# Kernel optimization log

Hardware: AMD Instinct MI355X
Metric: run time of the kernel (lower is better)

The kernel has to match this reference:

```python
import jax, jax.numpy as jnp
import numpy as np

N_NODES = 10000
N_PAIRS = 200000
NUM_FEATURES = 384
DEGREES = [1, 2, 3]
NHEADS = len(DEGREES)
F_HEAD = NUM_FEATURES // NHEADS  # 128
REPEATS = np.array([2 * d + 1 for d in DEGREES])  # [3,5,7]
SPH_DIM = int(REPEATS.sum())  # 15


def setup_inputs() -> dict:
    key = jax.random.key(0)
    ks = jax.random.split(key, 10)
    return {
        "chi": jax.random.normal(ks[0], (N_NODES, SPH_DIM), dtype=jnp.float32),
        "sph_ij": jax.random.normal(ks[1], (N_PAIRS, SPH_DIM), dtype=jnp.float32),
        "x": jax.random.normal(ks[2], (N_NODES, NUM_FEATURES), dtype=jnp.float32),
        "w_ij": jax.random.normal(ks[3], (N_PAIRS, NUM_FEATURES), dtype=jnp.float32),
        "idx_i": jax.random.randint(ks[4], (N_PAIRS,), 0, N_NODES),
        "phi_r_cut": jax.random.uniform(ks[5], (N_PAIRS, 1), dtype=jnp.float32),
        "phi_chi_cut": jax.random.uniform(ks[6], (N_PAIRS,), dtype=jnp.float32),
        "idx_j": jax.random.randint(ks[7], (N_PAIRS,), 0, N_NODES),
        # per-head linear weights (nn.Linear stores (out, in); y = x @ W.T)
        "Wq": jax.random.normal(ks[8], (NHEADS, F_HEAD, F_HEAD), dtype=jnp.float32) / np.sqrt(F_HEAD),
        "Wk": jax.random.normal(ks[9], (NHEADS, F_HEAD, F_HEAD), dtype=jnp.float32) / np.sqrt(F_HEAD),
    }


def reference(chi, sph_ij, x, w_ij, idx_i, phi_r_cut, phi_chi_cut, idx_j, Wq, Wk):
    n = x.shape[0]
    # split into heads: (n, H, Fh) / (E, H, Fh)
    x_h = x.reshape(n, NHEADS, F_HEAD)
    w_h = w_ij.reshape(-1, NHEADS, F_HEAD)
    # per-head linears (vmapped Linear, no bias): y = x @ W.T
    q = jnp.einsum("nhf,hgf->nhg", x_h, Wq)  # (n, H, Fh)
    k = jnp.einsum("nhf,hgf->nhg", x_h, Wk)  # (n, H, Fh)
    # gather + elementwise attention coefficients per head: (E, H)
    alpha = (q[idx_i] * w_h * k[idx_j]).sum(-1) / np.sqrt(F_HEAD).astype(np.float32)
    # combine radial and sphc cutoffs
    alpha = alpha * phi_r_cut + alpha * phi_chi_cut[:, None]  # (E, H)
    # repeat each head over its 2l+1 spherical components -> (E, SPH_DIM)
    alpha_rep = jnp.repeat(alpha, REPEATS, axis=-1, total_repeat_length=SPH_DIM)
    # scatter-add messages into center atoms -> (n, SPH_DIM)
    chi_ = jax.ops.segment_sum(alpha_rep * sph_ij, idx_i, num_segments=n)
    return chi_
```

## Files before the change

### kernel.cpp

```cpp
#include <hip/hip_runtime.h>
#include <hip/hip_bf16.h>
#include <hip/hip_fp16.h>

#define N_NODES 10000
#define N_PAIRS 200000
#define NFEAT 384
#define FH 128
#define SPH 15

typedef __bf16 bf16x8 __attribute__((ext_vector_type(8)));
typedef _Float16 half8 __attribute__((ext_vector_type(8)));
typedef float f32x4 __attribute__((ext_vector_type(4)));

__device__ inline bf16x8 cvt8(const float* __restrict__ p) {
    float4 lo = *(const float4*)p;
    float4 hi = *(const float4*)(p + 4);
    bf16x8 r;
    r[0] = (__bf16)lo.x; r[1] = (__bf16)lo.y; r[2] = (__bf16)lo.z; r[3] = (__bf16)lo.w;
    r[4] = (__bf16)hi.x; r[5] = (__bf16)hi.y; r[6] = (__bf16)hi.z; r[7] = (__bf16)hi.w;
    return r;
}

__global__ __launch_bounds__(256) void qk_gemm_kernel(
        const float* __restrict__ x,
        const float* __restrict__ Wq,
        const float* __restrict__ Wk,
        _Float16* __restrict__ q, _Float16* __restrict__ k) {
    const int head = blockIdx.y;
    const int node0 = blockIdx.x * 16;
    const int wave = threadIdx.x >> 6;
    const int lane = threadIdx.x & 63;
    const int mrow = lane & 15;
    const int quad = lane >> 4;
    const float* xrow = x + (size_t)(node0 + mrow) * NFEAT + head * FH + quad * 8;
    bf16x8 afrag[4];
#pragma unroll
    for (int t = 0; t < 4; ++t) afrag[t] = cvt8(xrow + t * 32);

    for (int task = wave; task < 16; task += 4) {
        const int mat = task & 1;
        const int g0 = (task >> 1) * 16;
        const float* Wrow =
            (mat ? Wk : Wq) + (size_t)head * FH * FH + (size_t)(g0 + mrow) * FH + quad * 8;
        f32x4 acc = {0.f, 0.f, 0.f, 0.f};
#pragma unroll
        for (int t = 0; t < 4; ++t) {
            bf16x8 b = cvt8(Wrow + t * 32);
            acc = __builtin_amdgcn_mfma_f32_16x16x32_bf16(afrag[t], b, acc, 0, 0, 0);
        }
        _Float16* dst = mat ? k : q;
        const int g = g0 + mrow;
#pragma unroll
        for (int r = 0; r < 4; ++r) {
            const int node = node0 + quad * 4 + r;
            dst[(size_t)node * NFEAT + head * FH + g] = (_Float16)acc[r];
        }
    }
}

__global__ __launch_bounds__(256) void pair_kernel(
        const _Float16* __restrict__ q, const _Float16* __restrict__ kk,
        const float* __restrict__ w_ij, const float* __restrict__ sph,
        const int* __restrict__ idx_i, const int* __restrict__ idx_j,
        const float* __restrict__ phi_r, const float* __restrict__ phi_chi,
        float* __restrict__ out) {
    const int lane = threadIdx.x & 63;
    const int sub = lane & 15;
    const int grp = lane >> 4;
    const int wid = blockIdx.x * (blockDim.x >> 6) + (threadIdx.x >> 6);
    const int nw = gridDim.x * (blockDim.x >> 6);
    for (int base = wid * 4; base < N_PAIRS; base += nw * 4) {
        const int e = base + grp;
        if (e < N_PAIRS) {
            const int i = idx_i[e];
            const int j = idx_j[e];
            const _Float16* qr = q + (size_t)i * NFEAT;
            const _Float16* kr = kk + (size_t)j * NFEAT;
            const float* wr = w_ij + (size_t)e * NFEAT;
            float dot[3];
#pragma unroll
            for (int h = 0; h < 3; ++h) {
                const int f = h * FH + sub * 8;
                half8 qv = *(const half8*)(qr + f);
                half8 kv = *(const half8*)(kr + f);
                f32x4 wa = __builtin_nontemporal_load((const f32x4*)(wr + f));
                f32x4 wb = __builtin_nontemporal_load((const f32x4*)(wr + f + 4));
                float p = 0.f;
#pragma unroll
                for (int u = 0; u < 4; ++u) {
                    p = fmaf((float)qv[u] * wa[u], (float)kv[u], p);
                    p = fmaf((float)qv[u + 4] * wb[u], (float)kv[u + 4], p);
                }
#pragma unroll
                for (int off = 8; off; off >>= 1) p += __shfl_xor(p, off, 16);
                dot[h] = p;
            }
            const float pr = __builtin_nontemporal_load(phi_r + e);
            const float pc = __builtin_nontemporal_load(phi_chi + e);
            const float scale = (pr + pc) * 0.088388347648318447f;
            if (sub < SPH) {
                const int h = (sub < 3) ? 0 : (sub < 8 ? 1 : 2);
                const float s = __builtin_nontemporal_load(sph + (size_t)e * SPH + sub);
                const float val = dot[h] * scale * s;
                unsafeAtomicAdd(&out[(size_t)i * SPH + sub], val);
            }
        }
    }
}

extern "C" void kernel_launch(void* const* d_in, const int* in_sizes, int n_in,
                              void* d_out, int out_size, void* d_ws, size_t ws_size,
                              hipStream_t stream) {
    const float* sph     = (const float*)d_in[1];
    const float* x       = (const float*)d_in[2];
    const float* w_ij    = (const float*)d_in[3];
    const int*   idx_i   = (const int*)d_in[4];
    const float* phi_r   = (const float*)d_in[5];
    const float* phi_chi = (const float*)d_in[6];
    const int*   idx_j   = (const int*)d_in[7];
    const float* Wq      = (const float*)d_in[8];
    const float* Wk      = (const float*)d_in[9];
    float* out = (float*)d_out;

    char* ws = (char*)d_ws;
    _Float16* qws = (_Float16*)ws;
    _Float16* kws = (_Float16*)(ws + 7680000);

    hipMemsetAsync(d_out, 0, (size_t)out_size * sizeof(float), stream);

    qk_gemm_kernel<<<dim3(N_NODES / 16, 3), 256, 0, stream>>>(x, Wq, Wk, qws, kws);

    pair_kernel<<<2048, 256, 0, stream>>>(qws, kws, w_ij, sph, idx_i, idx_j,
                                          phi_r, phi_chi, out);
}
```

Before: 482.1 us.

## Replace atomic scatter with CSR-sorted per-node gather and register accumulation

Builds a CSR grouping of pairs by destination node (count, scan, scatter into a permutation) every call, then processes each node with one wave. The q row stays in registers and the 15 outputs are reduced in-wave with a single plain store. This removes per-pair float atomics and repeated q gathers. The cost is three extra small kernels, including a single-block scan, a random-order read of w_ij through the permutation that hurts coalescing, and load imbalance from variable node degrees.

```diff
diff --git a/kernel.cpp b/kernel.cpp
--- a/kernel.cpp
+++ b/kernel.cpp
@@ -58,54 +58,115 @@
     }
 }
 
-__global__ __launch_bounds__(256) void pair_kernel(
+__global__ __launch_bounds__(256) void count_kernel(const int* __restrict__ idx_i,
+                                                    int* __restrict__ cnt) {
+    for (int e = blockIdx.x * blockDim.x + threadIdx.x; e < N_PAIRS;
+         e += gridDim.x * blockDim.x)
+        atomicAdd(&cnt[idx_i[e]], 1);
+}
+
+__global__ __launch_bounds__(1024) void scan_kernel(const int* __restrict__ cnt,
+                                                    int* __restrict__ starts,
+                                                    int* __restrict__ cursor) {
+    __shared__ int lds[1024];
+    const int tid = threadIdx.x;
+    const int base = tid * 10;
+    int pref[10];
+    int s = 0;
+#pragma unroll
+    for (int t = 0; t < 10; ++t) {
+        int v = (base + t < N_NODES) ? cnt[base + t] : 0;
+        pref[t] = s;
+        s += v;
+    }
+    lds[tid] = s;
+    __syncthreads();
+    for (int off = 1; off < 1024; off <<= 1) {
+        int v = (tid >= off) ? lds[tid - off] : 0;
+        __syncthreads();
+        lds[tid] += v;
+        __syncthreads();
+    }
+    const int excl = tid ? lds[tid - 1] : 0;
+#pragma unroll
+    for (int t = 0; t < 10; ++t) {
+        if (base + t < N_NODES) {
+            const int v = excl + pref[t];
+            starts[base + t] = v;
+            cursor[base + t] = v;
+        }
+    }
+}
+
+__global__ __launch_bounds__(256) void scatter_kernel(const int* __restrict__ idx_i,
+                                                      int* __restrict__ cursor,
+                                                      int* __restrict__ perm) {
+    for (int e = blockIdx.x * blockDim.x + threadIdx.x; e < N_PAIRS;
+         e += gridDim.x * blockDim.x) {
+        const int i = idx_i[e];
+        const int pos = atomicAdd(&cursor[i], 1);
+        perm[pos] = e;
+    }
+}
+
+__global__ __launch_bounds__(256) void node_kernel(
         const _Float16* __restrict__ q, const _Float16* __restrict__ kk,
         const float* __restrict__ w_ij, const float* __restrict__ sph,
-        const int* __restrict__ idx_i, const int* __restrict__ idx_j,
+        const int* __restrict__ perm, const int* __restrict__ starts,
+        const int* __restrict__ cnt, const int* __restrict__ idx_j,
         const float* __restrict__ phi_r, const float* __restrict__ phi_chi,
         float* __restrict__ out) {
     const int lane = threadIdx.x & 63;
     const int sub = lane & 15;
     const int grp = lane >> 4;
-    const int wid = blockIdx.x * (blockDim.x >> 6) + (threadIdx.x >> 6);
-    const int nw = gridDim.x * (blockDim.x >> 6);
-    for (int base = wid * 4; base < N_PAIRS; base += nw * 4) {
-        const int e = base + grp;
-        if (e < N_PAIRS) {
-            const int i = idx_i[e];
-            const int j = idx_j[e];
-            const _Float16* qr = q + (size_t)i * NFEAT;
-            const _Float16* kr = kk + (size_t)j * NFEAT;
-            const float* wr = w_ij + (size_t)e * NFEAT;
-            float dot[3];
-#pragma unroll
-            for (int h = 0; h < 3; ++h) {
-                const int f = h * FH + sub * 8;
-                half8 qv = *(const half8*)(qr + f);
-                half8 kv = *(const half8*)(kr + f);
-                f32x4 wa = __builtin_nontemporal_load((const f32x4*)(wr + f));
-                f32x4 wb = __builtin_nontemporal_load((const f32x4*)(wr + f + 4));
-                float p = 0.f;
-#pragma unroll
-                for (int u = 0; u < 4; ++u) {
-                    p = fmaf((float)qv[u] * wa[u], (float)kv[u], p);
-                    p = fmaf((float)qv[u + 4] * wb[u], (float)kv[u + 4], p);
-                }
-#pragma unroll
-                for (int off = 8; off; off >>= 1) p += __shfl_xor(p, off, 16);
-                dot[h] = p;
+    const int node = blockIdx.x * (blockDim.x >> 6) + (threadIdx.x >> 6);
+    if (node >= N_NODES) return;
+
+    const int start = starts[node];
+    const int end = start + cnt[node];
+
+    half8 qv[3];
+#pragma unroll
+    for (int h = 0; h < 3; ++h)
+        qv[h] = *(const half8*)(q + (size_t)node * NFEAT + h * FH + sub * 8);
+
+    float acc = 0.f;
+
+    for (int p = start + grp; p < end; p += 4) {
+        const int e = perm[p];
+        const int j = idx_j[e];
+        const _Float16* kr = kk + (size_t)j * NFEAT;
+        const float* wr = w_ij + (size_t)e * NFEAT;
+        float dot[3];
+#pragma unroll
+        for (int h = 0; h < 3; ++h) {
+            const int f = h * FH + sub * 8;
+            half8 kv = *(const half8*)(kr + f);
+            f32x4 wa = __builtin_nontemporal_load((const f32x4*)(wr + f));
+            f32x4 wb = __builtin_nontemporal_load((const f32x4*)(wr + f + 4));
+            float d = 0.f;
+#pragma unroll
+            for (int u = 0; u < 4; ++u) {
+                d = fmaf((float)qv[h][u] * wa[u], (float)kv[u], d);
+                d = fmaf((float)qv[h][u + 4] * wb[u], (float)kv[u + 4], d);
             }
-            const float pr = __builtin_nontemporal_load(phi_r + e);
-            const float pc = __builtin_nontemporal_load(phi_chi + e);
-            const float scale = (pr + pc) * 0.088388347648318447f;
-            if (sub < SPH) {
-                const int h = (sub < 3) ? 0 : (sub < 8 ? 1 : 2);
-                const float s = __builtin_nontemporal_load(sph + (size_t)e * SPH + sub);
-                const float val = dot[h] * scale * s;
-                unsafeAtomicAdd(&out[(size_t)i * SPH + sub], val);
-            }
-        }
-    }
+#pragma unroll
+            for (int off = 8; off; off >>= 1) d += __shfl_xor(d, off, 16);
+            dot[h] = d;
+        }
+        const float pr = __builtin_nontemporal_load(phi_r + e);
+        const float pc = __builtin_nontemporal_load(phi_chi + e);
+        const float scale = (pr + pc) * 0.088388347648318447f;
+        if (sub < SPH) {
+            const int h = (sub < 3) ? 0 : (sub < 8 ? 1 : 2);
+            const float sv = __builtin_nontemporal_load(sph + (size_t)e * SPH + sub);
+            acc = fmaf(dot[h] * scale, sv, acc);
+        }
+    }
+
+    acc += __shfl_xor(acc, 16);
+    acc += __shfl_xor(acc, 32);
+    if (grp == 0 && sub < SPH) out[(size_t)node * SPH + sub] = acc;
 }
 
 extern "C" void kernel_launch(void* const* d_in, const int* in_sizes, int n_in,
@@ -125,11 +186,18 @@
     char* ws = (char*)d_ws;
     _Float16* qws = (_Float16*)ws;
     _Float16* kws = (_Float16*)(ws + 7680000);
-
-    hipMemsetAsync(d_out, 0, (size_t)out_size * sizeof(float), stream);
+    int* cnt    = (int*)(ws + 15360000);
+    int* starts = (int*)(ws + 15400000);
+    int* cursor = (int*)(ws + 15440000);
+    int* perm   = (int*)(ws + 15480000);
+
+    hipMemsetAsync(cnt, 0, N_NODES * sizeof(int), stream);
+    count_kernel<<<256, 256, 0, stream>>>(idx_i, cnt);
+    scan_kernel<<<1, 1024, 0, stream>>>(cnt, starts, cursor);
+    scatter_kernel<<<256, 256, 0, stream>>>(idx_i, cursor, perm);
 
     qk_gemm_kernel<<<dim3(N_NODES / 16, 3), 256, 0, stream>>>(x, Wq, Wk, qws, kws);
 
-    pair_kernel<<<2048, 256, 0, stream>>>(qws, kws, w_ij, sph, idx_i, idx_j,
-                                          phi_r, phi_chi, out);
-}
+    node_kernel<<<(N_NODES + 3) / 4, 256, 0, stream>>>(
+        qws, kws, w_ij, sph, perm, starts, cnt, idx_j, phi_r, phi_chi, out);
+}
```

New measurement: 530.1 us. 1.1x slower.
